# Performance work log

Measured on AMD Instinct MI355X. Metric: run time of the kernel, lower is better.

The kernel has to match this reference:

```python
import jax, jax.numpy as jnp
import numpy as np
import math

B, H, S, D = 8, 16, 1024, 64

def setup_inputs() -> dict:
    key = jax.random.key(0)
    kq, kk, kv, km = jax.random.split(key, 4)
    queries = jax.random.normal(kq, (B, H, S, D), dtype=jnp.float32)
    keys = jax.random.normal(kk, (B, H, S, D), dtype=jnp.float32)
    values = jax.random.normal(kv, (B, H, S, D), dtype=jnp.float32)
    mask = jax.random.randint(km, (B, 1, S, S), 0, 2, dtype=jnp.int32)
    return {"queries": queries, "keys": keys, "values": values, "mask": mask}

def reference(queries, keys, values, mask):
    d = values.shape[3]
    # scores: [B,H,S,S] = Q @ K^T / sqrt(d)
    scores = jnp.einsum('bhqd,bhkd->bhqk', queries, keys) / math.sqrt(d)
    attn = jax.nn.softmax(scores, axis=-1)
    # Faithful to source: mask applied AFTER softmax via masked_fill(mask==0, -100000)
    attn = jnp.where(mask == 0, jnp.float32(-100000.0), attn)
    out = jnp.einsum('bhqk,bhkd->bhqd', attn, values)
    return (out, attn)
```

## Files before the change

kernel.cpp:

```cpp
#include <hip/hip_runtime.h>

constexpr int Bm = 8, Hm = 16, Sm = 1024, Dm = 64;
constexpr int BH = Bm * Hm;
constexpr int NBLK = BH * (Sm / 16);
constexpr int STRIDE = 1040;

typedef short short8  __attribute__((ext_vector_type(8)));
typedef float floatx4 __attribute__((ext_vector_type(4)));
typedef int   intx4   __attribute__((ext_vector_type(4)));

__device__ inline unsigned short f2bf(float f) {
    unsigned u = __builtin_bit_cast(unsigned, f);
    u += 0x7fffu + ((u >> 16) & 1u);
    return (unsigned short)(u >> 16);
}
__device__ inline float bf2f(unsigned short h) {
    unsigned u = ((unsigned)h) << 16;
    return __builtin_bit_cast(float, u);
}

__global__ __launch_bounds__(256, 4)
void attn_fused(const float* __restrict__ Q, const float* __restrict__ K,
                const float* __restrict__ V, const int* __restrict__ Msk,
                float* __restrict__ Out, float* __restrict__ Attn)
{
    __shared__ __align__(16) unsigned short strip[16 * STRIDE];

    const int tid  = threadIdx.x;
    const int wave = tid >> 6;
    const int lane = tid & 63;
    const int quad = lane >> 4;
    const int ln   = lane & 15;

    const int bid = (blockIdx.x & 7) * (NBLK >> 3) + (blockIdx.x >> 3);
    const int bh = bid >> 6;
    const int qt = bid & 63;
    const int q0 = qt << 4;
    const int b  = bh >> 4;

    const float* Qb = Q + (size_t)bh * (Sm * Dm);
    const float* Kb = K + (size_t)bh * (Sm * Dm);
    const float* Vb = V + (size_t)bh * (Sm * Dm);

    short8 aq0, aq1;
    {
        const float* qrow = Qb + (q0 + ln) * Dm + quad * 8;
        floatx4 a = *(const floatx4*)(qrow);
        floatx4 c = *(const floatx4*)(qrow + 4);
        floatx4 d = *(const floatx4*)(qrow + 32);
        floatx4 e = *(const floatx4*)(qrow + 36);
        #pragma unroll
        for (int i = 0; i < 4; ++i) {
            aq0[i]     = (short)f2bf(a[i] * 0.125f);
            aq0[i + 4] = (short)f2bf(c[i] * 0.125f);
            aq1[i]     = (short)f2bf(d[i] * 0.125f);
            aq1[i + 4] = (short)f2bf(e[i] * 0.125f);
        }
    }

    for (int kt = wave * 16; kt < wave * 16 + 16; ++kt) {
        const float* krow = Kb + (kt * 16 + ln) * Dm + quad * 8;
        floatx4 k0 = *(const floatx4*)(krow);
        floatx4 k1 = *(const floatx4*)(krow + 4);
        floatx4 k2 = *(const floatx4*)(krow + 32);
        floatx4 k3 = *(const floatx4*)(krow + 36);
        short8 b0, b1;
        #pragma unroll
        for (int i = 0; i < 4; ++i) {
            b0[i]     = (short)f2bf(k0[i]);
            b0[i + 4] = (short)f2bf(k1[i]);
            b1[i]     = (short)f2bf(k2[i]);
            b1[i + 4] = (short)f2bf(k3[i]);
        }
        floatx4 c = {0.f, 0.f, 0.f, 0.f};
        c = __builtin_amdgcn_mfma_f32_16x16x32_bf16(aq0, b0, c, 0, 0, 0);
        c = __builtin_amdgcn_mfma_f32_16x16x32_bf16(aq1, b1, c, 0, 0, 0);
        const int colb = kt * 16 + ln;
        #pragma unroll
        for (int r = 0; r < 4; ++r)
            strip[(quad * 4 + r) * STRIDE + colb] = f2bf(c[r]);
    }
    __syncthreads();

    {
        const int row = tid >> 4, l = tid & 15;
        unsigned short* srow = strip + row * STRIDE;

        float mx = -1e30f;
        #pragma unroll
        for (int i = 0; i < 8; ++i) {
            short8 v = *(const short8*)(srow + l * 8 + i * 128);
            #pragma unroll
            for (int j = 0; j < 8; ++j) mx = fmaxf(mx, bf2f((unsigned short)v[j]));
        }
        #pragma unroll
        for (int off = 8; off >= 1; off >>= 1) mx = fmaxf(mx, __shfl_xor(mx, off, 16));

        float sum = 0.f;
        #pragma unroll
        for (int i = 0; i < 8; ++i) {
            short8 v = *(const short8*)(srow + l * 8 + i * 128);
            short8 e;
            #pragma unroll
            for (int j = 0; j < 8; ++j) {
                float x = __expf(bf2f((unsigned short)v[j]) - mx);
                sum += x;
                e[j] = (short)f2bf(x);
            }
            *(short8*)(srow + l * 8 + i * 128) = e;
        }
        #pragma unroll
        for (int off = 8; off >= 1; off >>= 1) sum += __shfl_xor(sum, off, 16);
        const float rn = 1.f / sum;

        const int* mrow  = Msk + (size_t)b * (Sm * Sm) + (size_t)(q0 + row) * Sm;
        float*     arow  = Attn + ((size_t)bh * Sm + (q0 + row)) * Sm;
        #pragma unroll
        for (int i = 0; i < 8; ++i) {
            const int c0 = l * 8 + i * 128;
            short8 v  = *(const short8*)(srow + c0);
            intx4  m0 = *(const intx4*)(mrow + c0);
            intx4  m1 = *(const intx4*)(mrow + c0 + 4);
            float p[8];
            #pragma unroll
            for (int j = 0; j < 4; ++j) {
                p[j]     = (m0[j] != 0) ? bf2f((unsigned short)v[j])     * rn : -100000.f;
                p[j + 4] = (m1[j] != 0) ? bf2f((unsigned short)v[j + 4]) * rn : -100000.f;
            }
            floatx4 o0, o1;
            short8 pf;
            #pragma unroll
            for (int j = 0; j < 4; ++j) { o0[j] = p[j]; o1[j] = p[j + 4]; }
            #pragma unroll
            for (int j = 0; j < 8; ++j) pf[j] = (short)f2bf(p[j]);
            *(short8*)(srow + c0) = pf;
            *(floatx4*)(arow + c0)     = o0;
            *(floatx4*)(arow + c0 + 4) = o1;
        }
    }
    __syncthreads();

    floatx4 acc[4] = {{0,0,0,0},{0,0,0,0},{0,0,0,0},{0,0,0,0}};
    for (int kb = wave * 256; kb < wave * 256 + 256; kb += 32) {
        short8 af = *(const short8*)(strip + ln * STRIDE + kb + quad * 8);
        const float* vbase = Vb + (kb + quad * 8) * Dm + ln;
        #pragma unroll
        for (int n0 = 0; n0 < 4; ++n0) {
            short8 bf;
            #pragma unroll
            for (int j = 0; j < 8; ++j)
                bf[j] = (short)f2bf(vbase[j * Dm + n0 * 16]);
            acc[n0] = __builtin_amdgcn_mfma_f32_16x16x32_bf16(af, bf, acc[n0], 0, 0, 0);
        }
    }
    __syncthreads();

    float* part = (float*)strip;
    #pragma unroll
    for (int n0 = 0; n0 < 4; ++n0)
        #pragma unroll
        for (int r = 0; r < 4; ++r)
            part[wave * 1024 + (quad * 4 + r) * 64 + n0 * 16 + ln] = acc[n0][r];
    __syncthreads();
    {
        const int o4 = tid * 4;
        floatx4 s = *(const floatx4*)(part + o4);
        s += *(const floatx4*)(part + 1024 + o4);
        s += *(const floatx4*)(part + 2048 + o4);
        s += *(const floatx4*)(part + 3072 + o4);
        const int row = o4 >> 6, dc = o4 & 63;
        *(floatx4*)(Out + (size_t)bh * (Sm * Dm) + (size_t)(q0 + row) * Dm + dc) = s;
    }
}

extern "C" void kernel_launch(void* const* d_in, const int* in_sizes, int n_in,
                              void* d_out, int out_size, void* d_ws, size_t ws_size,
                              hipStream_t stream)
{
    const float* Q   = (const float*)d_in[0];
    const float* K   = (const float*)d_in[1];
    const float* V   = (const float*)d_in[2];
    const int*   Msk = (const int*)d_in[3];
    float* Out  = (float*)d_out;
    float* Attn = Out + (size_t)Bm * Hm * Sm * Dm;

    attn_fused<<<dim3(NBLK), dim3(256), 0, stream>>>(Q, K, V, Msk, Out, Attn);
}
```

Before: 945.0 us.

## Preconvert K to bf16 and V to transposed bf16 in a prepass kernel

Adds a prepass kernel that converts K to bf16 and writes V as a transposed bf16 array into the workspace. The main kernel then loads MFMA operands directly as 16-byte vectors instead of converting fp32 values per block, which each of the 64 q-tile blocks per head previously repeated. This also replaces the strided scalar V gathers with contiguous loads. It costs an extra launch and a workspace round trip, and falls back to the old kernel when the workspace is too small.

```diff
diff --git a/kernel.cpp b/kernel.cpp
--- a/kernel.cpp
+++ b/kernel.cpp
@@ -19,10 +19,216 @@
     return __builtin_bit_cast(float, u);
 }
 
+__global__ __launch_bounds__(256)
+void preconv(const float* __restrict__ K, const float* __restrict__ V,
+             unsigned short* __restrict__ Kbf, unsigned short* __restrict__ VT)
+{
+    __shared__ unsigned short tile[64][72];
+
+    const int blk = blockIdx.x;
+    const int bh  = blk >> 4;
+    const int t   = blk & 15;
+    const int tid = threadIdx.x;
+    const int row = tid >> 2;
+    const int c0  = (tid & 3) << 4;
+
+    {
+        const float* src = K + ((size_t)bh * Sm + t * 64 + row) * Dm + c0;
+        unsigned short* dst = Kbf + ((size_t)bh * Sm + t * 64 + row) * Dm + c0;
+        floatx4 a0 = *(const floatx4*)(src);
+        floatx4 a1 = *(const floatx4*)(src + 4);
+        floatx4 a2 = *(const floatx4*)(src + 8);
+        floatx4 a3 = *(const floatx4*)(src + 12);
+        short8 p0, p1;
+        #pragma unroll
+        for (int i = 0; i < 4; ++i) {
+            p0[i]     = (short)f2bf(a0[i]);
+            p0[i + 4] = (short)f2bf(a1[i]);
+            p1[i]     = (short)f2bf(a2[i]);
+            p1[i + 4] = (short)f2bf(a3[i]);
+        }
+        *(short8*)(dst)     = p0;
+        *(short8*)(dst + 8) = p1;
+    }
+
+    {
+        const float* src = V + ((size_t)bh * Sm + t * 64 + row) * Dm + c0;
+        floatx4 a0 = *(const floatx4*)(src);
+        floatx4 a1 = *(const floatx4*)(src + 4);
+        floatx4 a2 = *(const floatx4*)(src + 8);
+        floatx4 a3 = *(const floatx4*)(src + 12);
+        short8 p0, p1;
+        #pragma unroll
+        for (int i = 0; i < 4; ++i) {
+            p0[i]     = (short)f2bf(a0[i]);
+            p0[i + 4] = (short)f2bf(a1[i]);
+            p1[i]     = (short)f2bf(a2[i]);
+            p1[i + 4] = (short)f2bf(a3[i]);
+        }
+        *(short8*)(&tile[row][c0])     = p0;
+        *(short8*)(&tile[row][c0 + 8]) = p1;
+    }
+    __syncthreads();
+    {
+        const int drow = tid >> 2;
+        const int kc0  = (tid & 3) << 4;
+        unsigned short* dst = VT + ((size_t)bh * Dm + drow) * Sm + t * 64 + kc0;
+        short8 p0, p1;
+        #pragma unroll
+        for (int j = 0; j < 8; ++j) {
+            p0[j] = (short)tile[kc0 + j][drow];
+            p1[j] = (short)tile[kc0 + 8 + j][drow];
+        }
+        *(short8*)(dst)     = p0;
+        *(short8*)(dst + 8) = p1;
+    }
+}
+
 __global__ __launch_bounds__(256, 4)
-void attn_fused(const float* __restrict__ Q, const float* __restrict__ K,
-                const float* __restrict__ V, const int* __restrict__ Msk,
+void attn_fused(const float* __restrict__ Q, const unsigned short* __restrict__ Kbf,
+                const unsigned short* __restrict__ VT, const int* __restrict__ Msk,
                 float* __restrict__ Out, float* __restrict__ Attn)
+{
+    __shared__ __align__(16) unsigned short strip[16 * STRIDE];
+
+    const int tid  = threadIdx.x;
+    const int wave = tid >> 6;
+    const int lane = tid & 63;
+    const int quad = lane >> 4;
+    const int ln   = lane & 15;
+
+    const int bid = (blockIdx.x & 7) * (NBLK >> 3) + (blockIdx.x >> 3);
+    const int bh = bid >> 6;
+    const int qt = bid & 63;
+    const int q0 = qt << 4;
+    const int b  = bh >> 4;
+
+    const float* Qb = Q + (size_t)bh * (Sm * Dm);
+    const unsigned short* Kb = Kbf + (size_t)bh * (Sm * Dm);
+    const unsigned short* Vb = VT + (size_t)bh * (Dm * Sm);
+
+    short8 aq0, aq1;
+    {
+        const float* qrow = Qb + (q0 + ln) * Dm + quad * 8;
+        floatx4 a = *(const floatx4*)(qrow);
+        floatx4 c = *(const floatx4*)(qrow + 4);
+        floatx4 d = *(const floatx4*)(qrow + 32);
+        floatx4 e = *(const floatx4*)(qrow + 36);
+        #pragma unroll
+        for (int i = 0; i < 4; ++i) {
+            aq0[i]     = (short)f2bf(a[i] * 0.125f);
+            aq0[i + 4] = (short)f2bf(c[i] * 0.125f);
+            aq1[i]     = (short)f2bf(d[i] * 0.125f);
+            aq1[i + 4] = (short)f2bf(e[i] * 0.125f);
+        }
+    }
+
+    for (int kt = wave * 16; kt < wave * 16 + 16; ++kt) {
+        const unsigned short* krow = Kb + (kt * 16 + ln) * Dm + quad * 8;
+        short8 b0 = *(const short8*)(krow);
+        short8 b1 = *(const short8*)(krow + 32);
+        floatx4 c = {0.f, 0.f, 0.f, 0.f};
+        c = __builtin_amdgcn_mfma_f32_16x16x32_bf16(aq0, b0, c, 0, 0, 0);
+        c = __builtin_amdgcn_mfma_f32_16x16x32_bf16(aq1, b1, c, 0, 0, 0);
+        const int colb = kt * 16 + ln;
+        #pragma unroll
+        for (int r = 0; r < 4; ++r)
+            strip[(quad * 4 + r) * STRIDE + colb] = f2bf(c[r]);
+    }
+    __syncthreads();
+
+    {
+        const int row = tid >> 4, l = tid & 15;
+        unsigned short* srow = strip + row * STRIDE;
+
+        float mx = -1e30f;
+        #pragma unroll
+        for (int i = 0; i < 8; ++i) {
+            short8 v = *(const short8*)(srow + l * 8 + i * 128);
+            #pragma unroll
+            for (int j = 0; j < 8; ++j) mx = fmaxf(mx, bf2f((unsigned short)v[j]));
+        }
+        #pragma unroll
+        for (int off = 8; off >= 1; off >>= 1) mx = fmaxf(mx, __shfl_xor(mx, off, 16));
+
+        float sum = 0.f;
+        #pragma unroll
+        for (int i = 0; i < 8; ++i) {
+            short8 v = *(const short8*)(srow + l * 8 + i * 128);
+            short8 e;
+            #pragma unroll
+            for (int j = 0; j < 8; ++j) {
+                float x = __expf(bf2f((unsigned short)v[j]) - mx);
+                sum += x;
+                e[j] = (short)f2bf(x);
+            }
+            *(short8*)(srow + l * 8 + i * 128) = e;
+        }
+        #pragma unroll
+        for (int off = 8; off >= 1; off >>= 1) sum += __shfl_xor(sum, off, 16);
+        const float rn = 1.f / sum;
+
+        const int* mrow  = Msk + (size_t)b * (Sm * Sm) + (size_t)(q0 + row) * Sm;
+        float*     arow  = Attn + ((size_t)bh * Sm + (q0 + row)) * Sm;
+        #pragma unroll
+        for (int i = 0; i < 8; ++i) {
+            const int c0 = l * 8 + i * 128;
+            short8 v  = *(const short8*)(srow + c0);
+            intx4  m0 = *(const intx4*)(mrow + c0);
+            intx4  m1 = *(const intx4*)(mrow + c0 + 4);
+            float p[8];
+            #pragma unroll
+            for (int j = 0; j < 4; ++j) {
+                p[j]     = (m0[j] != 0) ? bf2f((unsigned short)v[j])     * rn : -100000.f;
+                p[j + 4] = (m1[j] != 0) ? bf2f((unsigned short)v[j + 4]) * rn : -100000.f;
+            }
+            floatx4 o0, o1;
+            short8 pf;
+            #pragma unroll
+            for (int j = 0; j < 4; ++j) { o0[j] = p[j]; o1[j] = p[j + 4]; }
+            #pragma unroll
+            for (int j = 0; j < 8; ++j) pf[j] = (short)f2bf(p[j]);
+            *(short8*)(srow + c0) = pf;
+            *(floatx4*)(arow + c0)     = o0;
+            *(floatx4*)(arow + c0 + 4) = o1;
+        }
+    }
+    __syncthreads();
+
+    floatx4 acc[4] = {{0,0,0,0},{0,0,0,0},{0,0,0,0},{0,0,0,0}};
+    for (int kb = wave * 256; kb < wave * 256 + 256; kb += 32) {
+        short8 af = *(const short8*)(strip + ln * STRIDE + kb + quad * 8);
+        const unsigned short* vbase = Vb + kb + quad * 8;
+        #pragma unroll
+        for (int n0 = 0; n0 < 4; ++n0) {
+            short8 bf = *(const short8*)(vbase + (size_t)(n0 * 16 + ln) * Sm);
+            acc[n0] = __builtin_amdgcn_mfma_f32_16x16x32_bf16(af, bf, acc[n0], 0, 0, 0);
+        }
+    }
+    __syncthreads();
+
+    float* part = (float*)strip;
+    #pragma unroll
+    for (int n0 = 0; n0 < 4; ++n0)
+        #pragma unroll
+        for (int r = 0; r < 4; ++r)
+            part[wave * 1024 + (quad * 4 + r) * 64 + n0 * 16 + ln] = acc[n0][r];
+    __syncthreads();
+    {
+        const int o4 = tid * 4;
+        floatx4 s = *(const floatx4*)(part + o4);
+        s += *(const floatx4*)(part + 1024 + o4);
+        s += *(const floatx4*)(part + 2048 + o4);
+        s += *(const floatx4*)(part + 3072 + o4);
+        const int row = o4 >> 6, dc = o4 & 63;
+        *(floatx4*)(Out + (size_t)bh * (Sm * Dm) + (size_t)(q0 + row) * Dm + dc) = s;
+    }
+}
+
+__global__ __launch_bounds__(256, 4)
+void attn_fused_f32(const float* __restrict__ Q, const float* __restrict__ K,
+                    const float* __restrict__ V, const int* __restrict__ Msk,
+                    float* __restrict__ Out, float* __restrict__ Attn)
 {
     __shared__ __align__(16) unsigned short strip[16 * STRIDE];
 
@@ -184,5 +390,15 @@
     float* Out  = (float*)d_out;
     float* Attn = Out + (size_t)Bm * Hm * Sm * Dm;
 
-    attn_fused<<<dim3(NBLK), dim3(256), 0, stream>>>(Q, K, V, Msk, Out, Attn);
-}
+    const size_t nElem = (size_t)BH * Sm * Dm;
+    const size_t need  = nElem * 2 * sizeof(unsigned short);
+
+    if (d_ws != nullptr && ws_size >= need) {
+        unsigned short* Kbf = (unsigned short*)d_ws;
+        unsigned short* VT  = Kbf + nElem;
+        preconv<<<dim3(BH * 16), dim3(256), 0, stream>>>(K, V, Kbf, VT);
+        attn_fused<<<dim3(NBLK), dim3(256), 0, stream>>>(Q, Kbf, VT, Msk, Out, Attn);
+    } else {
+        attn_fused_f32<<<dim3(NBLK), dim3(256), 0, stream>>>(Q, K, V, Msk, Out, Attn);
+    }
+}
```

Measured after the change: 882.6 us. -6.6%, faster.
